# Kernel optimization log

Measured on AMD Instinct MI355X. Metric: run time of the kernel, lower is better.

## Reference

```python
import jax, jax.numpy as jnp
import numpy as np

G, C, L, D, H, NCLS = 64, 32, 128, 64, 128, 10


def setup_inputs() -> dict:
    key = jax.random.key(0)
    ks = jax.random.split(key, 5)
    scale = 0.05
    return {
        "cycle_reps": jax.random.normal(ks[0], (G, C, L, D), dtype=jnp.float32),
        "W_ih": jax.random.normal(ks[1], (4 * H, D), dtype=jnp.float32) * scale,
        "W_hh": jax.random.normal(ks[2], (4 * H, H), dtype=jnp.float32) * scale,
        "b_ih": jnp.zeros((4 * H,), dtype=jnp.float32),
        "b_hh": jnp.zeros((4 * H,), dtype=jnp.float32),
        "W_cls": jax.random.normal(ks[3], (NCLS, H), dtype=jnp.float32) * scale,
        "b_cls": jnp.zeros((NCLS,), dtype=jnp.float32),
    }


def _lstm_seq_sum(x, W_ih, W_hh, b):
    """Run a single-layer LSTM over x [B, L, D]; return sum of hidden states over L -> [B, H]."""
    B = x.shape[0]
    Hh = W_hh.shape[1]
    # precompute input-side gate pre-activations for all timesteps: [L, B, 4H]
    xg = jnp.einsum('bld,gd->lbg', x, W_ih) + b

    def step(carry, xg_t):
        h, c = carry
        gates = xg_t + h @ W_hh.T  # [B, 4H]
        i, f, g, o = jnp.split(gates, 4, axis=-1)  # torch i/f/g/o gate order
        i = jax.nn.sigmoid(i)
        f = jax.nn.sigmoid(f)
        g = jnp.tanh(g)
        o = jax.nn.sigmoid(o)
        c = f * c + i * g
        h = o * jnp.tanh(c)
        return (h, c), h

    init = (jnp.zeros((B, Hh), x.dtype), jnp.zeros((B, Hh), x.dtype))
    _, hs = jax.lax.scan(step, init, xg)  # hs: [L, B, H]
    return hs.sum(axis=0)


def reference(cycle_reps, W_ih, W_hh, b_ih, b_hh, W_cls, b_cls):
    Gn, Cn, Ln, Dn = cycle_reps.shape
    x = cycle_reps.reshape(Gn * Cn, Ln, Dn)
    rep = _lstm_seq_sum(x, W_ih, W_hh, b_ih + b_hh)  # [G*C, H]: sum of LSTM outputs over seq
    rep = rep.reshape(Gn, Cn, -1)
    # torch.var_mean over the cycle axis; only the mean is used as the graph rep
    graph_mean = rep.mean(axis=1)  # [G, H]
    logits = graph_mean @ W_cls.T + b_cls  # classifier_gnn
    return jax.nn.log_softmax(logits, axis=1)
```

## Files before the change

kernel.cpp:

```cpp
#include <hip/hip_runtime.h>
#include <hip/hip_bf16.h>

#define NSEQ 2048
#define LSEQ 128
#define DIN  64
#define HID  128
#define NCLS 10
#define XPAD 72
#define CHK  16

typedef __attribute__((ext_vector_type(8))) short bfrag8;
typedef __attribute__((ext_vector_type(4))) float facc4;

__device__ __forceinline__ short f2bf(float f) {
    union { __hip_bfloat16 b; short s; } u;
    u.b = __float2bfloat16(f);
    return u.s;
}

__device__ __forceinline__ bfrag8 load_bf16_frag(const float* __restrict__ p) {
    bfrag8 r;
#pragma unroll
    for (int j = 0; j < 8; ++j) r[j] = f2bf(p[j]);
    return r;
}

__device__ __forceinline__ float fast_sigmoid(float x) {
    float e = __builtin_amdgcn_exp2f(-1.4426950408889634f * x);
    return __builtin_amdgcn_rcpf(1.0f + e);
}
__device__ __forceinline__ float fast_tanh(float x) {
    float e = __builtin_amdgcn_exp2f(2.8853900817779268f * x);
    return 1.0f - 2.0f * __builtin_amdgcn_rcpf(1.0f + e);
}

__device__ __forceinline__ float lane_redistribute(float r_low, float r_high) {
    float d = r_low, s = r_high;
    asm("v_permlane32_swap_b32 %0, %1" : "+v"(d), "+v"(s));
    return d;
}

__global__ __launch_bounds__(512) void lstm_fused(
    const float* __restrict__ x,
    const float* __restrict__ Wih,
    const float* __restrict__ Whh,
    const float* __restrict__ bih,
    const float* __restrict__ bhh,
    float* __restrict__ rep)
{
    __shared__ __align__(16) __hip_bfloat16 hbuf[2][16][136];
    __shared__ __align__(16) __hip_bfloat16 xs[2][CHK][8][XPAD];

    const int tid  = threadIdx.x;
    const int w    = tid >> 6;
    const int lane = tid & 63;
    const int ln   = lane & 15;
    const int qd   = lane >> 4;
    const int s0   = blockIdx.x * 8;
    const int khid = w * 16 + ln;
    const int sq0  = (qd & 1) * 4 + (qd >> 1) * 2;
    const int sq1  = sq0 + 1;

    bfrag8 whh[4][4];
    bfrag8 wih[4][2];
    facc4  biasf[4];
#pragma unroll
    for (int g = 0; g < 4; ++g) {
        const int col = g * HID + khid;
        const float b = bih[col] + bhh[col];
        biasf[g] = (facc4){b, b, b, b};
#pragma unroll
        for (int k0 = 0; k0 < 4; ++k0)
            whh[g][k0] = load_bf16_frag(Whh + col * HID + k0 * 32 + qd * 8);
#pragma unroll
        for (int k0 = 0; k0 < 2; ++k0)
            wih[g][k0] = load_bf16_frag(Wih + col * DIN + k0 * 32 + qd * 8);
    }

    {
        unsigned int* p = (unsigned int*)&hbuf[0][0][0];
        for (int i = tid; i < 2 * 16 * 136 / 2; i += 512) p[i] = 0u;
    }

    const float* xsrc = x + (size_t)(s0 + w) * (LSEQ * DIN) + lane * 16;
    const int stt = lane >> 2;
    const int sdd = (lane & 3) * 16;

    {
        float4 a0 = ((const float4*)xsrc)[0];
        float4 a1 = ((const float4*)xsrc)[1];
        float4 a2 = ((const float4*)xsrc)[2];
        float4 a3 = ((const float4*)xsrc)[3];
        bfrag8 o0, o1;
#pragma unroll
        for (int j = 0; j < 4; ++j) { o0[j] = f2bf(((float*)&a0)[j]); o0[4+j] = f2bf(((float*)&a1)[j]); }
#pragma unroll
        for (int j = 0; j < 4; ++j) { o1[j] = f2bf(((float*)&a2)[j]); o1[4+j] = f2bf(((float*)&a3)[j]); }
        *(bfrag8*)&xs[0][stt][w][sdd]     = o0;
        *(bfrag8*)&xs[0][stt][w][sdd + 8] = o1;
    }

    float cst[2]  = {0.f, 0.f};
    float hsum[2] = {0.f, 0.f};

    __syncthreads();

    facc4 accA[4], accB[4];
    {
        bfrag8 x0 = *(const bfrag8*)(&xs[0][0][ln & 7][qd * 8]);
        bfrag8 x1 = *(const bfrag8*)(&xs[0][0][ln & 7][32 + qd * 8]);
#pragma unroll
        for (int g = 0; g < 4; ++g) {
            accA[g] = __builtin_amdgcn_mfma_f32_16x16x32_bf16(x0, wih[g][0], biasf[g], 0, 0, 0);
            accA[g] = __builtin_amdgcn_mfma_f32_16x16x32_bf16(x1, wih[g][1], accA[g], 0, 0, 0);
        }
    }

    int cur = 0;

#define STEP(ACCIN, ACCOUT, CT)                                                          \
    {                                                                                    \
        const int ct = (CT);                                                             \
                                             \
        bfrag8 hf[4];                                                                    \
        _Pragma("unroll")                                                                \
        for (int k0 = 0; k0 < 4; ++k0)                                                   \
            hf[k0] = *(const bfrag8*)(&hbuf[cur][ln][k0 * 32 + qd * 8]);                 \
             \
        const int nbuf = (ct < CHK - 1) ? buf : (buf ^ 1);                               \
        const int nct  = (ct + 1) & (CHK - 1);                                           \
        bfrag8 xf0 = *(const bfrag8*)(&xs[nbuf][nct][ln & 7][qd * 8]);                   \
        bfrag8 xf1 = *(const bfrag8*)(&xs[nbuf][nct][ln & 7][32 + qd * 8]);              \
                    \
        _Pragma("unroll")                                                                \
        for (int g = 0; g < 4; ++g)                                                      \
            _Pragma("unroll")                                                            \
            for (int k0 = 0; k0 < 4; ++k0)                                               \
                ACCIN[g] = __builtin_amdgcn_mfma_f32_16x16x32_bf16(hf[k0], whh[g][k0], ACCIN[g], 0, 0, 0); \
                        \
        float u0[4], u1[4];                                                              \
        _Pragma("unroll")                                                                \
        for (int g = 0; g < 4; ++g) {                                                    \
            u0[g] = lane_redistribute(ACCIN[g][0], ACCIN[g][2]);                         \
            u1[g] = lane_redistribute(ACCIN[g][1], ACCIN[g][3]);                         \
        }                                                                                \
                  \
        _Pragma("unroll")                                                                \
        for (int g = 0; g < 4; ++g) {                                                    \
            ACCOUT[g] = __builtin_amdgcn_mfma_f32_16x16x32_bf16(xf0, wih[g][0], biasf[g], 0, 0, 0); \
            ACCOUT[g] = __builtin_amdgcn_mfma_f32_16x16x32_bf16(xf1, wih[g][1], ACCOUT[g], 0, 0, 0); \
        }                                                                                \
        if (ct == 0 && more) {                      \
            const float* p = xsrc + (chunk + 1) * (CHK * DIN);                           \
            l0 = ((const float4*)p)[0];                                                  \
            l1 = ((const float4*)p)[1];                                                  \
            l2 = ((const float4*)p)[2];                                                  \
            l3 = ((const float4*)p)[3];                                                  \
        }                                                                                \
        if (ct == 12 && more) {                   \
            bfrag8 o0, o1;                                                               \
            _Pragma("unroll")                                                            \
            for (int j = 0; j < 4; ++j) { o0[j] = f2bf(((float*)&l0)[j]); o0[4+j] = f2bf(((float*)&l1)[j]); } \
            _Pragma("unroll")                                                            \
            for (int j = 0; j < 4; ++j) { o1[j] = f2bf(((float*)&l2)[j]); o1[4+j] = f2bf(((float*)&l3)[j]); } \
            *(bfrag8*)&xs[buf ^ 1][stt][w][sdd]     = o0;                                \
            *(bfrag8*)&xs[buf ^ 1][stt][w][sdd + 8] = o1;                                \
        }                                                                                \
                               \
        short hb[2];                                                                     \
        _Pragma("unroll")                                                                \
        for (int j = 0; j < 2; ++j) {                                                    \
            float iv = fast_sigmoid(j ? u1[0] : u0[0]);                                  \
            float fv = fast_sigmoid(j ? u1[1] : u0[1]);                                  \
            float gv = fast_tanh(j ? u1[2] : u0[2]);                                     \
            float ov = fast_sigmoid(j ? u1[3] : u0[3]);                                  \
            float c  = fv * cst[j] + iv * gv;                                            \
            cst[j]   = c;                                                                \
            float hv = ov * fast_tanh(c);                                                \
            hsum[j] += hv;                                                               \
            hb[j]    = f2bf(hv);                                                         \
        }                                                                                \
        ((short*)&hbuf[cur ^ 1][sq0][0])[khid] = hb[0];                                  \
        ((short*)&hbuf[cur ^ 1][sq1][0])[khid] = hb[1];                                  \
        __syncthreads();                                                                 \
        cur ^= 1;                                                                        \
    }

    for (int chunk = 0; chunk < LSEQ / CHK; ++chunk) {
        const int buf = chunk & 1;
        const bool more = chunk < (LSEQ / CHK - 1);
        float4 l0, l1, l2, l3;
#pragma unroll 1
        for (int ct2 = 0; ct2 < CHK / 2; ++ct2) {
            STEP(accA, accB, 2 * ct2);
            STEP(accB, accA, 2 * ct2 + 1);
        }
    }
#undef STEP

    rep[(size_t)(s0 + sq0) * HID + khid] = hsum[0];
    rep[(size_t)(s0 + sq1) * HID + khid] = hsum[1];
}

__global__ __launch_bounds__(128) void cls_kernel(
    const float* __restrict__ rep,
    const float* __restrict__ Wcls,
    const float* __restrict__ bcls,
    float* __restrict__ out)
{
    __shared__ float m_s[HID];
    __shared__ float logits_s[NCLS];
    const int g = blockIdx.x;
    const int h = threadIdx.x;

    float s = 0.f;
#pragma unroll 4
    for (int c = 0; c < 32; ++c)
        s += rep[((size_t)g * 32 + c) * HID + h];
    m_s[h] = s * (1.0f / 32.0f);
    __syncthreads();

    if (h < NCLS) {
        float acc = bcls[h];
        for (int k = 0; k < HID; ++k)
            acc += m_s[k] * Wcls[h * HID + k];
        logits_s[h] = acc;
    }
    __syncthreads();

    if (h < NCLS) {
        float mx = logits_s[0];
#pragma unroll
        for (int j = 1; j < NCLS; ++j) mx = fmaxf(mx, logits_s[j]);
        float se = 0.f;
#pragma unroll
        for (int j = 0; j < NCLS; ++j)
            se += __builtin_amdgcn_exp2f((logits_s[j] - mx) * 1.4426950408889634f);
        float lse = mx + 0.6931471805599453f * __builtin_amdgcn_logf(se);
        out[g * NCLS + h] = logits_s[h] - lse;
    }
}

extern "C" void kernel_launch(void* const* d_in, const int* in_sizes, int n_in,
                              void* d_out, int out_size, void* d_ws, size_t ws_size,
                              hipStream_t stream) {
    const float* x    = (const float*)d_in[0];
    const float* Wih  = (const float*)d_in[1];
    const float* Whh  = (const float*)d_in[2];
    const float* bih  = (const float*)d_in[3];
    const float* bhh  = (const float*)d_in[4];
    const float* Wcls = (const float*)d_in[5];
    const float* bcls = (const float*)d_in[6];

    float* rep = (float*)d_ws;

    lstm_fused<<<NSEQ / 8, 512, 0, stream>>>(x, Wih, Whh, bih, bhh, rep);
    cls_kernel<<<64, 128, 0, stream>>>(rep, Wcls, bcls, (float*)d_out);
}
```

Before: 200.5 us.

## Split recurrent MFMA chains, lighten barriers, atomically reduce graph sums

The recurrent gate MFMA chain of length four is split into two independent chains of two, summed afterward, which shortens the dependent MFMA latency on the serial critical path. __syncthreads is replaced by a barrier that waits only on LDS counters, so pending global loads no longer stall the step barrier. The per-sequence hidden sums are reduced across the block and atomically added into per-graph sums. This needs an extra zeroing kernel, and the classifier kernel now uses a wave-parallel dot product.

Measured after the change: 207.6 us. 3.6% more time.

```diff
diff --git a/kernel.cpp b/kernel.cpp
--- a/kernel.cpp
+++ b/kernel.cpp
@@ -40,13 +40,19 @@
     return d;
 }
 
+__device__ __forceinline__ void block_barrier() {
+    asm volatile("s_waitcnt lgkmcnt(0)" ::: "memory");
+    __builtin_amdgcn_s_barrier();
+    asm volatile("" ::: "memory");
+}
+
 __global__ __launch_bounds__(512) void lstm_fused(
     const float* __restrict__ x,
     const float* __restrict__ Wih,
     const float* __restrict__ Whh,
     const float* __restrict__ bih,
     const float* __restrict__ bhh,
-    float* __restrict__ rep)
+    float* __restrict__ graphsum)
 {
     __shared__ __align__(16) __hip_bfloat16 hbuf[2][16][136];
     __shared__ __align__(16) __hip_bfloat16 xs[2][CHK][8][XPAD];
@@ -103,7 +109,7 @@
     float cst[2]  = {0.f, 0.f};
     float hsum[2] = {0.f, 0.f};
 
-    __syncthreads();
+    block_barrier();
 
     facc4 accA[4], accB[4];
     {
@@ -116,6 +122,7 @@
         }
     }
 
+    const facc4 zero4 = {0.f, 0.f, 0.f, 0.f};
     int cur = 0;
 
 #define STEP(ACCIN, ACCOUT, CT)                                                          \
@@ -131,18 +138,22 @@
         const int nct  = (ct + 1) & (CHK - 1);                                           \
         bfrag8 xf0 = *(const bfrag8*)(&xs[nbuf][nct][ln & 7][qd * 8]);                   \
         bfrag8 xf1 = *(const bfrag8*)(&xs[nbuf][nct][ln & 7][32 + qd * 8]);              \
-                    \
-        _Pragma("unroll")                                                                \
-        for (int g = 0; g < 4; ++g)                                                      \
-            _Pragma("unroll")                                                            \
-            for (int k0 = 0; k0 < 4; ++k0)                                               \
-                ACCIN[g] = __builtin_amdgcn_mfma_f32_16x16x32_bf16(hf[k0], whh[g][k0], ACCIN[g], 0, 0, 0); \
+                      \
+        facc4 gt[4];                                                                     \
+        _Pragma("unroll")                                                                \
+        for (int g = 0; g < 4; ++g) {                                                    \
+            facc4 pa = __builtin_amdgcn_mfma_f32_16x16x32_bf16(hf[0], whh[g][0], ACCIN[g], 0, 0, 0); \
+            pa = __builtin_amdgcn_mfma_f32_16x16x32_bf16(hf[1], whh[g][1], pa, 0, 0, 0); \
+            facc4 pb = __builtin_amdgcn_mfma_f32_16x16x32_bf16(hf[2], whh[g][2], zero4, 0, 0, 0); \
+            pb = __builtin_amdgcn_mfma_f32_16x16x32_bf16(hf[3], whh[g][3], pb, 0, 0, 0); \
+            gt[g] = pa + pb;                                                             \
+        }                                                                                \
                         \
         float u0[4], u1[4];                                                              \
         _Pragma("unroll")                                                                \
         for (int g = 0; g < 4; ++g) {                                                    \
-            u0[g] = lane_redistribute(ACCIN[g][0], ACCIN[g][2]);                         \
-            u1[g] = lane_redistribute(ACCIN[g][1], ACCIN[g][3]);                         \
+            u0[g] = lane_redistribute(gt[g][0], gt[g][2]);                               \
+            u1[g] = lane_redistribute(gt[g][1], gt[g][3]);                               \
         }                                                                                \
                   \
         _Pragma("unroll")                                                                \
@@ -182,7 +193,7 @@
         }                                                                                \
         ((short*)&hbuf[cur ^ 1][sq0][0])[khid] = hb[0];                                  \
         ((short*)&hbuf[cur ^ 1][sq1][0])[khid] = hb[1];                                  \
-        __syncthreads();                                                                 \
+        block_barrier();                                                                 \
         cur ^= 1;                                                                        \
     }
 
@@ -198,37 +209,47 @@
     }
 #undef STEP
 
-    rep[(size_t)(s0 + sq0) * HID + khid] = hsum[0];
-    rep[(size_t)(s0 + sq1) * HID + khid] = hsum[1];
+    float v = hsum[0] + hsum[1];
+    v += __shfl_xor(v, 16);
+    v += __shfl_xor(v, 32);
+    if (qd == 0)
+        atomicAdd(&graphsum[(size_t)(blockIdx.x >> 2) * HID + khid], v);
+}
+
+__global__ __launch_bounds__(512) void zero_gs(float* __restrict__ gs)
+{
+    gs[blockIdx.x * 512 + threadIdx.x] = 0.f;
 }
 
 __global__ __launch_bounds__(128) void cls_kernel(
-    const float* __restrict__ rep,
+    const float* __restrict__ gs,
     const float* __restrict__ Wcls,
     const float* __restrict__ bcls,
     float* __restrict__ out)
 {
     __shared__ float m_s[HID];
     __shared__ float logits_s[NCLS];
-    const int g = blockIdx.x;
-    const int h = threadIdx.x;
-
-    float s = 0.f;
-#pragma unroll 4
-    for (int c = 0; c < 32; ++c)
-        s += rep[((size_t)g * 32 + c) * HID + h];
-    m_s[h] = s * (1.0f / 32.0f);
+    const int g    = blockIdx.x;
+    const int tid  = threadIdx.x;
+    const int lane = tid & 63;
+    const int w    = tid >> 6;
+
+    m_s[tid] = gs[(size_t)g * HID + tid] * (1.0f / 32.0f);
     __syncthreads();
 
-    if (h < NCLS) {
-        float acc = bcls[h];
-        for (int k = 0; k < HID; ++k)
-            acc += m_s[k] * Wcls[h * HID + k];
-        logits_s[h] = acc;
+#pragma unroll
+    for (int cc = 0; cc < 5; ++cc) {
+        const int cls = w * 5 + cc;
+        float p = m_s[lane] * Wcls[cls * HID + lane]
+                + m_s[lane + 64] * Wcls[cls * HID + lane + 64];
+#pragma unroll
+        for (int off = 32; off > 0; off >>= 1)
+            p += __shfl_xor(p, off);
+        if (lane == 0) logits_s[cls] = p + bcls[cls];
     }
     __syncthreads();
 
-    if (h < NCLS) {
+    if (tid < NCLS) {
         float mx = logits_s[0];
 #pragma unroll
         for (int j = 1; j < NCLS; ++j) mx = fmaxf(mx, logits_s[j]);
@@ -237,7 +258,7 @@
         for (int j = 0; j < NCLS; ++j)
             se += __builtin_amdgcn_exp2f((logits_s[j] - mx) * 1.4426950408889634f);
         float lse = mx + 0.6931471805599453f * __builtin_amdgcn_logf(se);
-        out[g * NCLS + h] = logits_s[h] - lse;
+        out[g * NCLS + tid] = logits_s[tid] - lse;
     }
 }
 
@@ -252,8 +273,9 @@
     const float* Wcls = (const float*)d_in[5];
     const float* bcls = (const float*)d_in[6];
 
-    float* rep = (float*)d_ws;
-
-    lstm_fused<<<NSEQ / 8, 512, 0, stream>>>(x, Wih, Whh, bih, bhh, rep);
-    cls_kernel<<<64, 128, 0, stream>>>(rep, Wcls, bcls, (float*)d_out);
-}
+    float* graphsum = (float*)d_ws;
+
+    zero_gs<<<16, 512, 0, stream>>>(graphsum);
+    lstm_fused<<<NSEQ / 8, 512, 0, stream>>>(x, Wih, Whh, bih, bhh, graphsum);
+    cls_kernel<<<64, 128, 0, stream>>>(graphsum, Wcls, bcls, (float*)d_out);
+}
```
